# Performance work log

Measured on AMD Instinct MI355X. Metric: run time of the kernel, lower is better.

## Reference

```python
import jax, jax.numpy as jnp
import numpy as np

K = 32
BN_EPS = 1e-5


def _fps(points, n_samples):
    # Sequential farthest point sampling; deterministic start at index 0
    # (torch version uses a random start; math otherwise identical).
    B, N, _ = points.shape

    def step(carry, _):
        dist_min, far = carry                                   # (B,N), (B,)
        c = jnp.take_along_axis(points, far[:, None, None].astype(jnp.int32) * jnp.ones((1, 1, 3), jnp.int32), axis=1)  # (B,1,3)
        d = jnp.sum((points - c) ** 2, axis=2)                  # (B,N)
        dist_min = jnp.minimum(dist_min, d)
        return (dist_min, jnp.argmax(dist_min, axis=1)), far

    init = (jnp.full((B, N), 1e10, points.dtype), jnp.zeros((B,), jnp.int64).astype(jnp.int32))
    _, cent = jax.lax.scan(step, init, None, length=n_samples)  # (n_samples, B)
    return cent.T                                               # (B, n_samples)


def _knn_idx(cntrds, pnts, k):
    # squared euclidean distance (same neighbor ordering as torch.cdist)
    d2 = (jnp.sum(cntrds ** 2, -1)[:, :, None]
          + jnp.sum(pnts ** 2, -1)[:, None, :]
          - 2.0 * jnp.einsum('bsc,bnc->bsn', cntrds, pnts))     # (B,ns,N)
    _, idx = jax.lax.top_k(-d2, k)                              # smallest-k
    return idx                                                  # (B,ns,k)


def _gather(x, idx):
    # x: (B,N,D), idx: (B,...) -> (B,...,D)
    return jax.vmap(lambda a, i: a[i])(x, idx)


def _conv1x1(x, w):
    # x: (B,Cin,ns,k), w: (Cout,Cin)
    return jnp.einsum('oc,bcnk->bonk', w, x)


def _bn_relu(x, g, b):
    # training-mode BatchNorm2d (biased variance over B,ns,k) + ReLU
    mean = jnp.mean(x, axis=(0, 2, 3), keepdims=True)
    var = jnp.var(x, axis=(0, 2, 3), keepdims=True)
    xh = (x - mean) * jax.lax.rsqrt(var + BN_EPS)
    return jax.nn.relu(xh * g[None, :, None, None] + b[None, :, None, None])


def setup_inputs() -> dict:
    key = jax.random.key(0)
    ks = jax.random.split(key, 16)
    B, N = 4, 4096
    s = 0.05
    return {
        'p': jax.random.normal(ks[0], (B, N, 3), jnp.float32),
        'f': jax.random.normal(ks[1], (B, 3, N), jnp.float32),
        'w1': jax.random.normal(ks[2], (256, 6), jnp.float32) * s,
        'w2': jax.random.normal(ks[3], (256, 256), jnp.float32) * s,
        'b2': jax.random.normal(ks[4], (256,), jnp.float32) * s,
        'g2': jnp.ones((256,), jnp.float32),
        'be2': jnp.zeros((256,), jnp.float32),
        'w3': jax.random.normal(ks[5], (512, 512), jnp.float32) * s,
        'g3': jnp.ones((512,), jnp.float32),
        'be3': jnp.zeros((512,), jnp.float32),
        'w4': jax.random.normal(ks[6], (256, 512), jnp.float32) * s,
        'g4': jnp.ones((256,), jnp.float32),
        'be4': jnp.zeros((256,), jnp.float32),
    }


def reference(p, f, w1, w2, b2, g2, be2, w3, g3, be3, w4, g4, be4):
    B, N, _ = p.shape
    ns = N // 4
    idx_c = _fps(p, ns)                                   # (B,ns)
    cntrd = _gather(p, idx_c)                             # (B,ns,3)
    feats = jnp.transpose(f, (0, 2, 1))                   # (B,N,3)
    knn = _knn_idx(cntrd, p, K)                           # (B,ns,K)
    dp = _gather(p, knn)                                  # (B,ns,K,3)
    fj = _gather(feats, knn)                              # (B,ns,K,3)
    x = jnp.transpose(jnp.concatenate([dp, fj], -1), (0, 3, 1, 2))  # (B,6,ns,K)
    # conv1: 6->256 (no bias), 256->256 (bias) + BN + ReLU
    x = _conv1x1(x, w1)
    x = _conv1x1(x, w2) + b2[None, :, None, None]
    x = _bn_relu(x, g2, be2)                              # (B,256,ns,K)
    xm = jnp.max(x, axis=-1, keepdims=True)
    x = jnp.concatenate([jnp.broadcast_to(xm, x.shape), x], axis=1)  # (B,512,ns,K)
    # conv2: 512->512 BN ReLU, 512->256 BN ReLU
    x = _bn_relu(_conv1x1(x, w3), g3, be3)
    x = _bn_relu(_conv1x1(x, w4), g4, be4)
    out_feat = jnp.max(x, axis=-1)                        # (B,256,ns)
    return cntrd, out_feat
```

## Files before the change

kernel.cpp:

```cpp
#include <hip/hip_runtime.h>
#include <hip/hip_bf16.h>

#define B_ 4
#define N_ 4096
#define NS_ 1024
#define KNN_ 32
#define NPOS_ 131072
#define BN_EPS_ 1e-5f

using bf16 = __hip_bfloat16;
typedef unsigned short us;
typedef __attribute__((ext_vector_type(8))) short short8;
typedef __attribute__((ext_vector_type(4))) float f32x4;
typedef unsigned long long ull;

__device__ __forceinline__ float bf2f(bf16 h){ return __bfloat162float(h); }
__device__ __forceinline__ us f2bfbits(float x){
    bf16 h = __float2bfloat16(x);
    return *reinterpret_cast<us*>(&h);
}
__device__ __forceinline__ float bits2f(us u){
    unsigned v = ((unsigned)u)<<16; return __uint_as_float(v);
}
__device__ __forceinline__ void unpack8(uint4 v, float* f){
    f[0]=__uint_as_float((v.x&0xFFFFu)<<16); f[1]=__uint_as_float(v.x&0xFFFF0000u);
    f[2]=__uint_as_float((v.y&0xFFFFu)<<16); f[3]=__uint_as_float(v.y&0xFFFF0000u);
    f[4]=__uint_as_float((v.z&0xFFFFu)<<16); f[5]=__uint_as_float(v.z&0xFFFF0000u);
    f[6]=__uint_as_float((v.w&0xFFFFu)<<16); f[7]=__uint_as_float(v.w&0xFFFF0000u);
}
__device__ __forceinline__ uint4 pack8(const float* f){
    uint4 v;
    v.x = (unsigned)f2bfbits(f[0]) | ((unsigned)f2bfbits(f[1])<<16);
    v.y = (unsigned)f2bfbits(f[2]) | ((unsigned)f2bfbits(f[3])<<16);
    v.z = (unsigned)f2bfbits(f[4]) | ((unsigned)f2bfbits(f[5])<<16);
    v.w = (unsigned)f2bfbits(f[6]) | ((unsigned)f2bfbits(f[7])<<16);
    return v;
}
__device__ __forceinline__ unsigned fmono(float v){
    unsigned u = __float_as_uint(v);
    return (u & 0x80000000u) ? ~u : (u | 0x80000000u);
}

template<int CTRL, int ROWM>
__device__ __forceinline__ float dppmaxf(float x){
    int xi = __float_as_int(x);
    int yi = __builtin_amdgcn_update_dpp(xi, xi, CTRL, ROWM, 0xF, false);
    return fmaxf(x, __int_as_float(yi));
}
template<int CTRL, int ROWM>
__device__ __forceinline__ float dppminf(float x){
    int xi = __float_as_int(x);
    int yi = __builtin_amdgcn_update_dpp(xi, xi, CTRL, ROWM, 0xF, false);
    return fminf(x, __int_as_float(yi));
}
__device__ __forceinline__ float wave_max_f32(float x){
    x = dppmaxf<0x111,0xF>(x);
    x = dppmaxf<0x112,0xF>(x);
    x = dppmaxf<0x114,0xF>(x);
    x = dppmaxf<0x118,0xF>(x);
    x = dppmaxf<0x142,0xA>(x);
    x = dppmaxf<0x143,0xC>(x);
    return __int_as_float(__builtin_amdgcn_readlane(__float_as_int(x), 63));
}
__device__ __forceinline__ float wave_min_f32(float x){
    x = dppminf<0x111,0xF>(x);
    x = dppminf<0x112,0xF>(x);
    x = dppminf<0x114,0xF>(x);
    x = dppminf<0x118,0xF>(x);
    x = dppminf<0x142,0xA>(x);
    x = dppminf<0x143,0xC>(x);
    return __int_as_float(__builtin_amdgcn_readlane(__float_as_int(x), 63));
}
__device__ __forceinline__ float rowsum16(float x){
    x += __int_as_float(__builtin_amdgcn_update_dpp(0, __float_as_int(x), 0x111, 0xF, 0xF, true));
    x += __int_as_float(__builtin_amdgcn_update_dpp(0, __float_as_int(x), 0x112, 0xF, 0xF, true));
    x += __int_as_float(__builtin_amdgcn_update_dpp(0, __float_as_int(x), 0x114, 0xF, 0xF, true));
    x += __int_as_float(__builtin_amdgcn_update_dpp(0, __float_as_int(x), 0x118, 0xF, 0xF, true));
    return x;
}
__device__ __forceinline__ float max16(const float* v){
    float a = fmaxf(fmaxf(fmaxf(v[0],v[1]),v[2]),v[3]);
    float b = fmaxf(fmaxf(fmaxf(v[4],v[5]),v[6]),v[7]);
    float c = fmaxf(fmaxf(fmaxf(v[8],v[9]),v[10]),v[11]);
    float d = fmaxf(fmaxf(fmaxf(v[12],v[13]),v[14]),v[15]);
    return fmaxf(fmaxf(a,b), fmaxf(c,d));
}
__device__ __forceinline__ float min16(const float* v){
    float a = fminf(fminf(fminf(v[0],v[1]),v[2]),v[3]);
    float b = fminf(fminf(fminf(v[4],v[5]),v[6]),v[7]);
    float c = fminf(fminf(fminf(v[8],v[9]),v[10]),v[11]);
    float d = fminf(fminf(fminf(v[12],v[13]),v[14]),v[15]);
    return fminf(fminf(a,b), fminf(c,d));
}

#define NSLOT 64

__global__ __launch_bounds__(256) void bn_coef(const float* __restrict__ part,
                                               const float* __restrict__ g,
                                               const float* __restrict__ be,
                                               int chbase, int C,
                                               float2* __restrict__ ab){
    int c = blockIdx.x*256 + threadIdx.x;
    if (c < C){
        const float* ps = part + (size_t)(chbase+c)*2*NSLOT;
        float s = 0.f, q = 0.f;
        #pragma unroll 8
        for (int i=0;i<NSLOT;i++){ s += ps[i]; q += ps[NSLOT+i]; }
        const float inv = 1.0f/(float)NPOS_;
        float mean = s*inv;
        float var  = q*inv - mean*mean;
        float a = g[c]*rsqrtf(var + BN_EPS_);
        ab[c] = make_float2(a, be[c] - mean*a);
    }
}

__global__ __launch_bounds__(256) void mega_kernel(const float* __restrict__ p,
                                                   const float* __restrict__ f,
                                                   float* __restrict__ cntrd,
                                                   float* __restrict__ part,
                                                   int* __restrict__ prog,
                                                   int* __restrict__ w26flag,
                                                   const float* __restrict__ w1,
                                                   const float* __restrict__ w2,
                                                   float* __restrict__ W26,
                                                   const float* __restrict__ b2,
                                                   const float* __restrict__ w3,
                                                   us* __restrict__ whi3,
                                                   const float* __restrict__ w4,
                                                   us* __restrict__ whi4,
                                                   bf16* __restrict__ z2){
    __shared__ float4 pxyz[N_];
    __shared__ ull warr[2][4];
    __shared__ int knnS[32];
    __shared__ float Ws[6][256];
    __shared__ float xs[6][32];
    __shared__ int ciS;
    const int bid = blockIdx.x;
    const int t = threadIdx.x;
    const int lane = t & 63;
    const int wave = t >> 6;

    if (bid < 4){
        const int b = bid;
        const float* pb = p + (size_t)b*N_*3;
        float rx[16], ry[16], rz[16], dist[16];
        #pragma unroll
        for (int j=0;j<16;j++){
            int i = t*16+j;
            float x = pb[i*3+0];
            float y = pb[i*3+1];
            float z = pb[i*3+2];
            rx[j]=x; ry[j]=y; rz[j]=z;
            pxyz[i] = make_float4(x,y,z,0.f);
            dist[j]=1e10f;
        }
        __syncthreads();
        float4 c = pxyz[0];
        if (t==0){
            atomicExch(&prog[b*NS_], 1);
            cntrd[(size_t)(b*NS_)*3+0] = c.x;
            cntrd[(size_t)(b*NS_)*3+1] = c.y;
            cntrd[(size_t)(b*NS_)*3+2] = c.z;
        }
        for (int s=1; s<NS_; s++){
            #pragma unroll
            for (int j=0;j<16;j++){
                float dx = __fsub_rn(rx[j],c.x);
                float dy = __fsub_rn(ry[j],c.y);
                float dz = __fsub_rn(rz[j],c.z);
                float d  = __fadd_rn(__fadd_rn(__fmul_rn(dx,dx),__fmul_rn(dy,dy)),__fmul_rn(dz,dz));
                dist[j] = fminf(dist[j], d);
            }
            float lmax = max16(dist);
            float wmax = wave_max_f32(lmax);
            unsigned msk = 0;
            #pragma unroll
            for (int j=0;j<16;j++) msk |= (dist[j]==wmax) ? (1u<<j) : 0u;
            ull ball = __ballot(msk != 0);
            int srclane = (int)__builtin_ctzll(ball);
            unsigned lmsk = (unsigned)__builtin_amdgcn_readlane((int)msk, srclane);
            int widx = (wave*64 + srclane)*16 + (int)__builtin_ctz(lmsk);
            if (lane==0)
                warr[s&1][wave] = ((ull)__float_as_uint(wmax)<<32) | (0xFFFFFFFFu - (unsigned)widx);
            __syncthreads();
            ull g0 = warr[s&1][0], g1 = warr[s&1][1], g2 = warr[s&1][2], g3 = warr[s&1][3];
            ull ga = g0 > g1 ? g0 : g1;
            ull gb = g2 > g3 ? g2 : g3;
            ull g  = ga > gb ? ga : gb;
            int cur = (int)(0xFFFFFFFFu - (unsigned)(g & 0xFFFFFFFFull));
            c = pxyz[cur];
            if (t==0){
                atomicExch(&prog[b*NS_+s], cur+1);
                cntrd[(size_t)(b*NS_+s)*3+0] = c.x;
                cntrd[(size_t)(b*NS_+s)*3+1] = c.y;
                cntrd[(size_t)(b*NS_+s)*3+2] = c.z;
            }
        }
        return;
    }
    if (bid == 4){
        float acc[6] = {0,0,0,0,0,0};
        for (int k=0;k<256;k++){
            float w2v = w2[t*256+k];
            #pragma unroll
            for (int j=0;j<6;j++) acc[j] = fmaf(w2v, w1[k*6+j], acc[j]);
        }
        #pragma unroll
        for (int j=0;j<6;j++) W26[j*256+t] = acc[j];
        __syncthreads();
        if (t==0){ __threadfence(); atomicExch(w26flag, 1); }
        return;
    }
    if (bid < 1029){
        int i = (bid-5)*256 + t;
        whi3[i] = f2bfbits(w3[i]);
        return;
    }
    if (bid < 1541){
        int i = (bid-1029)*256 + t;
        whi4[i] = f2bfbits(w4[i]);
        return;
    }
    const int wid = bid - 1541;
    const int b = wid & 3;
    const int si = wid >> 2;
    const int sidx = b*NS_ + si;
    const float* pb = p + (size_t)b*N_*3;
    if (t == 0){
        int v;
        while ((v = atomicAdd(&prog[sidx], 0)) == 0) {}
        ciS = v - 1;
    }
    __syncthreads();
    const int ci = ciS;
    float cx = pb[ci*3+0];
    float cy = pb[ci*3+1];
    float cz = pb[ci*3+2];
    float c2 = __fadd_rn(__fadd_rn(__fmul_rn(cx,cx),__fmul_rn(cy,cy)),__fmul_rn(cz,cz));
    float d2[16];
    #pragma unroll
    for (int j=0;j<16;j++){
        int i = t*16+j;
        float x = pb[i*3+0];
        float y = pb[i*3+1];
        float z = pb[i*3+2];
        float p2 = __fadd_rn(__fadd_rn(__fmul_rn(x,x),__fmul_rn(y,y)),__fmul_rn(z,z));
        float dot= __fadd_rn(__fadd_rn(__fmul_rn(cx,x),__fmul_rn(cy,y)),__fmul_rn(cz,z));
        d2[j] = __fsub_rn(__fadd_rn(c2,p2), __fmul_rn(2.0f,dot));
    }
    for (int it=0; it<KNN_; it++){
        float lmin = min16(d2);
        float wmin = wave_min_f32(lmin);
        unsigned msk = 0;
        #pragma unroll
        for (int j=0;j<16;j++) msk |= (d2[j]==wmin) ? (1u<<j) : 0u;
        ull ball = __ballot(msk != 0);
        int srclane = (int)__builtin_ctzll(ball);
        unsigned lmsk = (unsigned)__builtin_amdgcn_readlane((int)msk, srclane);
        int widx = (wave*64 + srclane)*16 + (int)__builtin_ctz(lmsk);
        if (lane==0)
            warr[it&1][wave] = ((ull)fmono(wmin)<<32) | (unsigned)widx;
        __syncthreads();
        ull g0 = warr[it&1][0], g1 = warr[it&1][1], g2 = warr[it&1][2], g3 = warr[it&1][3];
        ull ga = g0 < g1 ? g0 : g1;
        ull gb = g2 < g3 ? g2 : g3;
        ull g  = ga < gb ? ga : gb;
        int idx = (int)(g & 0xFFFFFFFFull);
        if ((idx>>4)==t) d2[idx & 15] = INFINITY;
        if (t==0) knnS[it] = idx;
    }
    if (t == 0){ while (atomicAdd(w26flag, 0) == 0) {} __threadfence(); }
    __syncthreads();
    #pragma unroll
    for (int r=0;r<6;r++) Ws[r][t] = W26[r*256+t];
    if (t < 32){
        int i = knnS[t];
        const float* fb = f + (size_t)b*3*N_;
        xs[0][t] = pb[i*3+0];
        xs[1][t] = pb[i*3+1];
        xs[2][t] = pb[i*3+2];
        xs[3][t] = fb[0*N_+i];
        xs[4][t] = fb[1*N_+i];
        xs[5][t] = fb[2*N_+i];
    }
    __syncthreads();
    float w0=Ws[0][t], w1v=Ws[1][t], w2v=Ws[2][t], w3v=Ws[3][t], w4v=Ws[4][t], w5v=Ws[5][t];
    float bias = b2[t];
    bf16* zrow = z2 + (size_t)t*NPOS_ + (size_t)sidx*KNN_;
    float ssum = 0.f, sq = 0.f;
    for (int k0=0;k0<32;k0+=8){
        float y[8];
        #pragma unroll
        for (int u=0;u<8;u++){
            int k = k0+u;
            float acc = bias;
            acc = fmaf(w0, xs[0][k], acc);
            acc = fmaf(w1v,xs[1][k], acc);
            acc = fmaf(w2v,xs[2][k], acc);
            acc = fmaf(w3v,xs[3][k], acc);
            acc = fmaf(w4v,xs[4][k], acc);
            acc = fmaf(w5v,xs[5][k], acc);
            float vr = bits2f(f2bfbits(acc));
            ssum += vr; sq = fmaf(vr, vr, sq);
            y[u] = acc;
        }
        *reinterpret_cast<uint4*>(zrow + k0) = pack8(y);
    }
    const int slot = wid & (NSLOT-1);
    atomicAdd(&part[(size_t)(t*2+0)*NSLOT + slot], ssum);
    atomicAdd(&part[(size_t)(t*2+1)*NSLOT + slot], sq);
}

__global__ __launch_bounds__(256) void xm_kernel(const bf16* __restrict__ z2raw,
                                                 const float2* __restrict__ ab,
                                                 bf16* __restrict__ xm){
    int gid = blockIdx.x*256 + threadIdx.x;
    int c = gid >> 12;
    int bs = gid & 4095;
    float2 s = ab[c];
    const uint4* xp = reinterpret_cast<const uint4*>(z2raw + (size_t)c*NPOS_ + (size_t)bs*KNN_);
    float m = 0.0f;
    #pragma unroll
    for (int r=0;r<4;r++){
        uint4 v = xp[r];
        float fv[8]; unpack8(v, fv);
        #pragma unroll
        for (int u=0;u<8;u++) m = fmaxf(m, fmaf(fv[u], s.x, s.y));
    }
    xm[(size_t)c*4096 + bs] = __float2bfloat16(m);
}

__global__ __launch_bounds__(256) void gemm128(const float* __restrict__ A, int lda, int aoff,
                                               const bf16* __restrict__ B,
                                               int M, int N, int K,
                                               float* __restrict__ Cf){
    __shared__ float As[16][128];
    __shared__ float Bs[16][128];
    const int tid = threadIdx.x;
    const int tx = tid & 15, ty = tid >> 4;
    const int m0 = blockIdx.y*128, n0 = blockIdx.x*128;
    float acc[8][8];
    #pragma unroll
    for (int i=0;i<8;i++)
        #pragma unroll
        for (int j=0;j<8;j++) acc[i][j]=0.f;
    const int arow = tid >> 1, akg = tid & 1;
    const int bkk = tid >> 4, bng = tid & 15;
    for (int k0=0;k0<K;k0+=16){
        const float* aptr = A + (size_t)(m0+arow)*lda + aoff + k0 + akg*8;
        float4 a0 = *reinterpret_cast<const float4*>(aptr);
        float4 a1 = *reinterpret_cast<const float4*>(aptr+4);
        As[akg*8+0][arow]=a0.x; As[akg*8+1][arow]=a0.y;
        As[akg*8+2][arow]=a0.z; As[akg*8+3][arow]=a0.w;
        As[akg*8+4][arow]=a1.x; As[akg*8+5][arow]=a1.y;
        As[akg*8+6][arow]=a1.z; As[akg*8+7][arow]=a1.w;
        uint4 bv = *reinterpret_cast<const uint4*>(B + (size_t)(k0+bkk)*N + n0 + bng*8);
        float bf[8]; unpack8(bv, bf);
        *reinterpret_cast<float4*>(&Bs[bkk][bng*8+0]) = make_float4(bf[0],bf[1],bf[2],bf[3]);
        *reinterpret_cast<float4*>(&Bs[bkk][bng*8+4]) = make_float4(bf[4],bf[5],bf[6],bf[7]);
        __syncthreads();
        #pragma unroll
        for (int kk=0;kk<16;kk++){
            float a[8], b[8];
            *reinterpret_cast<float4*>(&a[0]) = *reinterpret_cast<float4*>(&As[kk][ty*8+0]);
            *reinterpret_cast<float4*>(&a[4]) = *reinterpret_cast<float4*>(&As[kk][ty*8+4]);
            *reinterpret_cast<float4*>(&b[0]) = *reinterpret_cast<float4*>(&Bs[kk][tx*8+0]);
            *reinterpret_cast<float4*>(&b[4]) = *reinterpret_cast<float4*>(&Bs[kk][tx*8+4]);
            #pragma unroll
            for (int i=0;i<8;i++)
                #pragma unroll
                for (int j=0;j<8;j++)
                    acc[i][j] = fmaf(a[i], b[j], acc[i][j]);
        }
        __syncthreads();
    }
    const int n = n0 + tx*8;
    #pragma unroll
    for (int i=0;i<8;i++){
        int m = m0 + ty*8 + i;
        *reinterpret_cast<float4*>(Cf + (size_t)m*N + n + 0) = make_float4(acc[i][0],acc[i][1],acc[i][2],acc[i][3]);
        *reinterpret_cast<float4*>(Cf + (size_t)m*N + n + 4) = make_float4(acc[i][4],acc[i][5],acc[i][6],acc[i][7]);
    }
}

#define LDK 40
__global__ __launch_bounds__(256) void gemm_mfma(const us* __restrict__ Whi,
                                                 int ldw, int aoff,
                                                 const bf16* __restrict__ act, int K,
                                                 const float2* __restrict__ ab,
                                                 bf16* __restrict__ out,
                                                 const float* __restrict__ t3,
                                                 float* __restrict__ part, int chbase){
    __shared__ __align__(16) us AsH[128*LDK];
    __shared__ __align__(16) us Bs [128*LDK];
    __shared__ float t3s[128][4];
    const us* actu = reinterpret_cast<const us*>(act);
    const int t = threadIdx.x;
    const int m0 = blockIdx.x*128, n0 = blockIdx.y*128;
    const int wave = t>>6, lane = t&63;
    const int wm = wave>>1, wn = wave&1;
    const int q = lane>>4, col = lane&15;

    if (t3 && t < 128){
        const float* src = t3 + (size_t)(m0+t)*4096 + (n0>>5);
        t3s[t][0]=src[0]; t3s[t][1]=src[1]; t3s[t][2]=src[2]; t3s[t][3]=src[3];
    }

    f32x4 acc[4][4];
    #pragma unroll
    for (int i=0;i<4;i++)
        #pragma unroll
        for (int j=0;j<4;j++) acc[i][j] = (f32x4){0.f,0.f,0.f,0.f};

    const int ar = t>>1, ah = t&1;
    const int bn = t&127, bh = t>>7;

    for (int k0=0;k0<K;k0+=32){
        const us* sh = Whi + (size_t)(m0+ar)*ldw + aoff + k0 + ah*16;
        uint4 h0 = *reinterpret_cast<const uint4*>(sh);
        uint4 h1 = *reinterpret_cast<const uint4*>(sh+8);
        *reinterpret_cast<uint4*>(&AsH[ar*LDK + ah*16 + 0]) = h0;
        *reinterpret_cast<uint4*>(&AsH[ar*LDK + ah*16 + 8]) = h1;
        us bvals[16];
        #pragma unroll
        for (int j=0;j<16;j++){
            int k = k0 + bh*16 + j;
            float x = bits2f(actu[(size_t)k*NPOS_ + n0 + bn]);
            float2 s = ab[k];
            bvals[j] = f2bfbits(fmaxf(fmaf(x, s.x, s.y), 0.0f));
        }
        *reinterpret_cast<uint4*>(&Bs[bn*LDK + bh*16 + 0]) = *reinterpret_cast<uint4*>(&bvals[0]);
        *reinterpret_cast<uint4*>(&Bs[bn*LDK + bh*16 + 8]) = *reinterpret_cast<uint4*>(&bvals[8]);
        __syncthreads();
        short8 bf[4], afh[4];
        #pragma unroll
        for (int tn=0;tn<4;tn++)
            bf[tn] = *reinterpret_cast<const short8*>(&Bs[(wn*64+tn*16+col)*LDK + q*8]);
        #pragma unroll
        for (int tm=0;tm<4;tm++)
            afh[tm] = *reinterpret_cast<const short8*>(&AsH[(wm*64+tm*16+col)*LDK + q*8]);
        #pragma unroll
        for (int tm=0;tm<4;tm++)
            #pragma unroll
            for (int tn=0;tn<4;tn++)
                acc[tm][tn] = __builtin_amdgcn_mfma_f32_16x16x32_bf16(afh[tm], bf[tn], acc[tm][tn], 0, 0, 0);
        __syncthreads();
    }
    const int slot = (int)(blockIdx.y & (NSLOT-1));
    #pragma unroll
    for (int tm=0;tm<4;tm++){
        #pragma unroll
        for (int r=0;r<4;r++){
            int m_l = wm*64 + tm*16 + q*4 + r;
            float srow = 0.f, qrow = 0.f;
            #pragma unroll
            for (int tn=0;tn<4;tn++){
                int n_l = wn*64 + tn*16 + col;
                float vv = acc[tm][tn][r];
                if (t3) vv += t3s[m_l][n_l>>5];
                us hb = f2bfbits(vv);
                reinterpret_cast<us*>(out)[(size_t)(m0+m_l)*NPOS_ + n0 + n_l] = hb;
                float vr = bits2f(hb);
                srow += vr; qrow = fmaf(vr, vr, qrow);
            }
            srow = rowsum16(srow);
            qrow = rowsum16(qrow);
            if (col == 15){
                atomicAdd(&part[(size_t)((chbase + m0 + m_l)*2+0)*NSLOT + slot], srow);
                atomicAdd(&part[(size_t)((chbase + m0 + m_l)*2+1)*NSLOT + slot], qrow);
            }
        }
    }
}

__global__ __launch_bounds__(256) void final_kernel(const bf16* __restrict__ z4,
                                                    const float2* __restrict__ ab,
                                                    float* __restrict__ out){
    int gid = blockIdx.x*256 + threadIdx.x;
    int s = gid & 1023;
    int c = (gid >> 10) & 255;
    int b = gid >> 18;
    int bsi = b*NS_ + s;
    float2 sc = ab[c];
    const uint4* zp = reinterpret_cast<const uint4*>(z4 + (size_t)c*NPOS_ + (size_t)bsi*KNN_);
    float m = 0.0f;
    #pragma unroll
    for (int r=0;r<4;r++){
        uint4 v = zp[r];
        float fv[8]; unpack8(v, fv);
        #pragma unroll
        for (int u=0;u<8;u++) m = fmaxf(m, fmaf(fv[u], sc.x, sc.y));
    }
    out[(size_t)(b*256 + c)*NS_ + s] = m;
}

extern "C" void kernel_launch(void* const* d_in, const int* in_sizes, int n_in,
                              void* d_out, int out_size, void* d_ws, size_t ws_size,
                              hipStream_t stream) {
    const float* p   = (const float*)d_in[0];
    const float* f   = (const float*)d_in[1];
    const float* w1  = (const float*)d_in[2];
    const float* w2  = (const float*)d_in[3];
    const float* b2  = (const float*)d_in[4];
    const float* g2  = (const float*)d_in[5];
    const float* be2 = (const float*)d_in[6];
    const float* w3  = (const float*)d_in[7];
    const float* g3  = (const float*)d_in[8];
    const float* be3 = (const float*)d_in[9];
    const float* w4  = (const float*)d_in[10];
    const float* g4  = (const float*)d_in[11];
    const float* be4 = (const float*)d_in[12];

    char* ws = (char*)d_ws;
    float*  W26  = (float*)(ws + 540672);
    float2* ab2  = (float2*)(ws + 555008);
    float2* ab3  = (float2*)(ws + 557056);
    us* whi3 = (us*)(ws + 561152);
    us* whi4 = (us*)(ws + 1609728);
    float*  t3   = (float*)(ws + 2134016);
    bf16*   z2   = (bf16*)(ws + 10522624);
    bf16*   xm   = (bf16*)(ws + 77631488);
    bf16*   z3   = (bf16*)(ws + 79728640);
    float*  part = (float*)(ws + 213946368);
    int*    prog = (int*)(ws + 214470656);
    int*    w26flag = (int*)(ws + 214487040);
    float2* ab4  = (float2*)(ws + 214487104);
    bf16*   z4   = z2;

    float* out_cntrd = (float*)d_out;
    float* out_feat  = (float*)d_out + (size_t)B_*NS_*3;

    hipMemsetAsync(ws + 213946368, 0, 540676, stream);
    mega_kernel<<<5637, 256, 0, stream>>>(p, f, out_cntrd, part, prog, w26flag,
                                          w1, w2, W26, b2,
                                          w3, whi3, w4, whi4, z2);
    bn_coef<<<1, 256, 0, stream>>>(part, g2, be2, 0, 256, ab2);
    xm_kernel<<<4096, 256, 0, stream>>>(z2, ab2, xm);
    gemm128<<<dim3(32,4), 256, 0, stream>>>(w3, 512, 0, xm, 512, 4096, 256, t3);
    gemm_mfma<<<dim3(4,1024), 256, 0, stream>>>(whi3, 512, 256, z2, 256, ab2, z3, t3, part, 256);
    bn_coef<<<2, 256, 0, stream>>>(part, g3, be3, 256, 512, ab3);
    gemm_mfma<<<dim3(2,1024), 256, 0, stream>>>(whi4, 512, 0, z3, 512, ab3, z4, nullptr, part, 768);
    bn_coef<<<1, 256, 0, stream>>>(part, g4, be4, 768, 256, ab4);
    final_kernel<<<4096, 256, 0, stream>>>(z4, ab4, out_feat);
}
```

Before: 1.059 ms.

## Fold BN coefficient reduction into xm/final kernels and pre-apply BN2 in place

Removes two bn_coef launches by having xm_kernel and final_kernel each reduce the per-channel partial sums themselves and compute the BN scale and shift in shared memory. xm_kernel now also writes the BN+ReLU-normalized z2 back in place, so the first gemm_mfma skips the per-element affine+ReLU when loading its B tile. The cost is redundant per-block coefficient computation and an extra write pass over z2, traded against fewer launches and cheaper GEMM tile loads.

```diff
diff --git a/kernel.cpp b/kernel.cpp
--- a/kernel.cpp
+++ b/kernel.cpp
@@ -77,6 +77,12 @@
     x += __int_as_float(__builtin_amdgcn_update_dpp(0, __float_as_int(x), 0x114, 0xF, 0xF, true));
     x += __int_as_float(__builtin_amdgcn_update_dpp(0, __float_as_int(x), 0x118, 0xF, 0xF, true));
     return x;
+}
+__device__ __forceinline__ float wave_sum_f32(float x){
+    x = rowsum16(x);
+    x += __int_as_float(__builtin_amdgcn_update_dpp(0, __float_as_int(x), 0x142, 0xA, 0xF, false));
+    x += __int_as_float(__builtin_amdgcn_update_dpp(0, __float_as_int(x), 0x143, 0xC, 0xF, false));
+    return __int_as_float(__builtin_amdgcn_readlane(__float_as_int(x), 63));
 }
 __device__ __forceinline__ float max16(const float* v){
     float a = fmaxf(fmaxf(fmaxf(v[0],v[1]),v[2]),v[3]);
@@ -311,21 +317,41 @@
     atomicAdd(&part[(size_t)(t*2+1)*NSLOT + slot], sq);
 }
 
-__global__ __launch_bounds__(256) void xm_kernel(const bf16* __restrict__ z2raw,
-                                                 const float2* __restrict__ ab,
+__global__ __launch_bounds__(256) void xm_kernel(bf16* __restrict__ z2,
+                                                 const float* __restrict__ part,
+                                                 const float* __restrict__ g2,
+                                                 const float* __restrict__ be2,
                                                  bf16* __restrict__ xm){
-    int gid = blockIdx.x*256 + threadIdx.x;
-    int c = gid >> 12;
-    int bs = gid & 4095;
-    float2 s = ab[c];
-    const uint4* xp = reinterpret_cast<const uint4*>(z2raw + (size_t)c*NPOS_ + (size_t)bs*KNN_);
+    __shared__ float abS[2];
+    const int c = blockIdx.x >> 4;
+    const int t = threadIdx.x;
+    const int bs = ((blockIdx.x & 15) << 8) | t;
+    if (t < 64){
+        float s = part[(size_t)(c*2+0)*NSLOT + t];
+        float q = part[(size_t)(c*2+1)*NSLOT + t];
+        s = wave_sum_f32(s);
+        q = wave_sum_f32(q);
+        if (t==0){
+            const float inv = 1.0f/(float)NPOS_;
+            float mean = s*inv;
+            float var  = q*inv - mean*mean;
+            float a = g2[c]*rsqrtf(var + BN_EPS_);
+            abS[0] = a; abS[1] = be2[c] - mean*a;
+        }
+    }
+    __syncthreads();
+    const float a = abS[0], bb = abS[1];
+    uint4* xp = reinterpret_cast<uint4*>(z2 + (size_t)c*NPOS_ + (size_t)bs*KNN_);
     float m = 0.0f;
     #pragma unroll
     for (int r=0;r<4;r++){
         uint4 v = xp[r];
         float fv[8]; unpack8(v, fv);
         #pragma unroll
-        for (int u=0;u<8;u++) m = fmaxf(m, fmaf(fv[u], s.x, s.y));
+        for (int u=0;u<8;u++) fv[u] = fmaxf(fmaf(fv[u], a, bb), 0.0f);
+        #pragma unroll
+        for (int u=0;u<8;u++) m = fmaxf(m, fv[u]);
+        xp[r] = pack8(fv);
     }
     xm[(size_t)c*4096 + bs] = __float2bfloat16(m);
 }
@@ -422,12 +448,20 @@
         *reinterpret_cast<uint4*>(&AsH[ar*LDK + ah*16 + 0]) = h0;
         *reinterpret_cast<uint4*>(&AsH[ar*LDK + ah*16 + 8]) = h1;
         us bvals[16];
-        #pragma unroll
-        for (int j=0;j<16;j++){
-            int k = k0 + bh*16 + j;
-            float x = bits2f(actu[(size_t)k*NPOS_ + n0 + bn]);
-            float2 s = ab[k];
-            bvals[j] = f2bfbits(fmaxf(fmaf(x, s.x, s.y), 0.0f));
+        if (ab){
+            #pragma unroll
+            for (int j=0;j<16;j++){
+                int k = k0 + bh*16 + j;
+                float x = bits2f(actu[(size_t)k*NPOS_ + n0 + bn]);
+                float2 s = ab[k];
+                bvals[j] = f2bfbits(fmaxf(fmaf(x, s.x, s.y), 0.0f));
+            }
+        } else {
+            #pragma unroll
+            for (int j=0;j<16;j++){
+                int k = k0 + bh*16 + j;
+                bvals[j] = actu[(size_t)k*NPOS_ + n0 + bn];
+            }
         }
         *reinterpret_cast<uint4*>(&Bs[bn*LDK + bh*16 + 0]) = *reinterpret_cast<uint4*>(&bvals[0]);
         *reinterpret_cast<uint4*>(&Bs[bn*LDK + bh*16 + 8]) = *reinterpret_cast<uint4*>(&bvals[8]);
@@ -474,14 +508,31 @@
 }
 
 __global__ __launch_bounds__(256) void final_kernel(const bf16* __restrict__ z4,
-                                                    const float2* __restrict__ ab,
+                                                    const float* __restrict__ part,
+                                                    const float* __restrict__ g4,
+                                                    const float* __restrict__ be4,
                                                     float* __restrict__ out){
-    int gid = blockIdx.x*256 + threadIdx.x;
-    int s = gid & 1023;
-    int c = (gid >> 10) & 255;
-    int b = gid >> 18;
-    int bsi = b*NS_ + s;
-    float2 sc = ab[c];
+    __shared__ float abS[2];
+    const int t = threadIdx.x;
+    const int c = (blockIdx.x >> 2) & 255;
+    const int b = blockIdx.x >> 10;
+    const int s = ((blockIdx.x & 3) << 8) | t;
+    if (t < 64){
+        float ss = part[(size_t)((768+c)*2+0)*NSLOT + t];
+        float qq = part[(size_t)((768+c)*2+1)*NSLOT + t];
+        ss = wave_sum_f32(ss);
+        qq = wave_sum_f32(qq);
+        if (t==0){
+            const float inv = 1.0f/(float)NPOS_;
+            float mean = ss*inv;
+            float var  = qq*inv - mean*mean;
+            float a = g4[c]*rsqrtf(var + BN_EPS_);
+            abS[0] = a; abS[1] = be4[c] - mean*a;
+        }
+    }
+    __syncthreads();
+    const float a = abS[0], bb = abS[1];
+    const int bsi = b*NS_ + s;
     const uint4* zp = reinterpret_cast<const uint4*>(z4 + (size_t)c*NPOS_ + (size_t)bsi*KNN_);
     float m = 0.0f;
     #pragma unroll
@@ -489,7 +540,7 @@
         uint4 v = zp[r];
         float fv[8]; unpack8(v, fv);
         #pragma unroll
-        for (int u=0;u<8;u++) m = fmaxf(m, fmaf(fv[u], sc.x, sc.y));
+        for (int u=0;u<8;u++) m = fmaxf(m, fmaf(fv[u], a, bb));
     }
     out[(size_t)(b*256 + c)*NS_ + s] = m;
 }
@@ -513,7 +564,6 @@
 
     char* ws = (char*)d_ws;
     float*  W26  = (float*)(ws + 540672);
-    float2* ab2  = (float2*)(ws + 555008);
     float2* ab3  = (float2*)(ws + 557056);
     us* whi3 = (us*)(ws + 561152);
     us* whi4 = (us*)(ws + 1609728);
@@ -524,7 +574,6 @@
     float*  part = (float*)(ws + 213946368);
     int*    prog = (int*)(ws + 214470656);
     int*    w26flag = (int*)(ws + 214487040);
-    float2* ab4  = (float2*)(ws + 214487104);
     bf16*   z4   = z2;
 
     float* out_cntrd = (float*)d_out;
@@ -534,12 +583,10 @@
     mega_kernel<<<5637, 256, 0, stream>>>(p, f, out_cntrd, part, prog, w26flag,
                                           w1, w2, W26, b2,
                                           w3, whi3, w4, whi4, z2);
-    bn_coef<<<1, 256, 0, stream>>>(part, g2, be2, 0, 256, ab2);
-    xm_kernel<<<4096, 256, 0, stream>>>(z2, ab2, xm);
+    xm_kernel<<<4096, 256, 0, stream>>>(z2, part, g2, be2, xm);
     gemm128<<<dim3(32,4), 256, 0, stream>>>(w3, 512, 0, xm, 512, 4096, 256, t3);
-    gemm_mfma<<<dim3(4,1024), 256, 0, stream>>>(whi3, 512, 256, z2, 256, ab2, z3, t3, part, 256);
+    gemm_mfma<<<dim3(4,1024), 256, 0, stream>>>(whi3, 512, 256, z2, 256, nullptr, z3, t3, part, 256);
     bn_coef<<<2, 256, 0, stream>>>(part, g3, be3, 256, 512, ab3);
     gemm_mfma<<<dim3(2,1024), 256, 0, stream>>>(whi4, 512, 0, z3, 512, ab3, z4, nullptr, part, 768);
-    bn_coef<<<1, 256, 0, stream>>>(part, g4, be4, 768, 256, ab4);
-    final_kernel<<<4096, 256, 0, stream>>>(z4, ab4, out_feat);
-}
+    final_kernel<<<4096, 256, 0, stream>>>(z4, part, g4, be4, out_feat);
+}
```

Measured after the change: 1.112 ms. +5.0%, slower.
